# Optimization experiments

Measured on AMD Instinct MI355X. Metric: run time of the kernel, lower is better.

## Reference

```python
import jax, jax.numpy as jnp
import numpy as np

D_MODEL = 1024
N_HEAD = 16
N_KV_HEAD = 4
D_K = D_MODEL // N_HEAD          # 64
N_REP = N_HEAD // N_KV_HEAD      # 4
B, S = 2, 2048


def setup_inputs() -> dict:
    key = jax.random.key(0)
    ks = jax.random.split(key, 7)
    scale = 1.0 / np.sqrt(D_MODEL)
    return {
        "q": jax.random.normal(ks[0], (B, S, D_MODEL), jnp.float32),
        "k": jax.random.normal(ks[1], (B, S, D_MODEL), jnp.float32),
        "v": jax.random.normal(ks[2], (B, S, D_MODEL), jnp.float32),
        # weights stored [in, out] (nn.Linear applies x @ W.T; we fold the transpose)
        "W_q": jax.random.normal(ks[3], (D_MODEL, N_HEAD * D_K), jnp.float32) * scale,
        "W_k": jax.random.normal(ks[4], (D_MODEL, N_KV_HEAD * D_K), jnp.float32) * scale,
        "W_v": jax.random.normal(ks[5], (D_MODEL, N_KV_HEAD * D_K), jnp.float32) * scale,
        "W_o": jax.random.normal(ks[6], (D_MODEL, D_MODEL), jnp.float32) * scale,
    }


def reference(q, k, v, W_q, W_k, W_v, W_o):
    batch, seq_q, _ = q.shape
    seq_k = k.shape[1]
    # projections -> [b, h, s, d]
    Q = (q @ W_q).reshape(batch, seq_q, N_HEAD, D_K).transpose(0, 2, 1, 3)
    K = (k @ W_k).reshape(batch, seq_k, N_KV_HEAD, D_K).transpose(0, 2, 1, 3)
    V = (v @ W_v).reshape(batch, seq_k, N_KV_HEAD, D_K).transpose(0, 2, 1, 3)
    # repeat each KV head n_rep times consecutively (matches expand+reshape)
    K = jnp.repeat(K, N_REP, axis=1)  # [b, n_head, seq_k, d_k]
    V = jnp.repeat(V, N_REP, axis=1)
    scores = jnp.einsum('bhqd,bhkd->bhqk', Q, K) / np.sqrt(D_K).astype(jnp.float32)
    attn = jax.nn.softmax(scores, axis=-1)
    out = jnp.einsum('bhqk,bhkd->bhqd', attn, V)  # [b, h, seq_q, d_k]
    out = out.transpose(0, 2, 1, 3).reshape(batch, seq_q, D_MODEL)
    return out @ W_o
```

## Files before the change

### kernel.cpp

```cpp
#include <hip/hip_runtime.h>
#include <hip/hip_bf16.h>
#include <stdint.h>

#define DEVINL __device__ __forceinline__

typedef unsigned short u16;
typedef __bf16 bf16x8 __attribute__((ext_vector_type(8)));
typedef float f32x4 __attribute__((ext_vector_type(4)));
typedef float f32x16 __attribute__((ext_vector_type(16)));
typedef unsigned short u16x8 __attribute__((ext_vector_type(8)));
typedef unsigned int u32x4 __attribute__((ext_vector_type(4)));

constexpr int BATCH = 2, SEQ = 2048, DM = 1024, NH = 16, NKVH = 4, DK = 64;
#define QSCALE 0.18033688f

DEVINL u16 f2bf(float f) {
    unsigned u = __builtin_bit_cast(unsigned, f);
    u += 0x7fffu + ((u >> 16) & 1u);
    return (u16)(u >> 16);
}

DEVINL unsigned pkbf(float a, float b) {
    unsigned r;
    asm("v_cvt_pk_bf16_f32 %0, %1, %2" : "=v"(r) : "v"(a), "v"(b));
    return r;
}
DEVINL void swap32(unsigned& a, unsigned& b) {
    asm("v_permlane32_swap_b32 %0, %1" : "+v"(a), "+v"(b));
}
DEVINL float fexp2(float x) {
    float r;
    asm("v_exp_f32 %0, %1" : "=v"(r) : "v"(x));
    return r;
}

DEVINL void gload16(const void* g, void* l) {
    __builtin_amdgcn_global_load_lds(
        (const __attribute__((address_space(1))) unsigned int*)g,
        (__attribute__((address_space(3))) unsigned int*)l, 16, 0, 0);
}

DEVINL bf16x8 ldfrag(const u16* p) { return *reinterpret_cast<const bf16x8*>(p); }

__global__ __launch_bounds__(256) void prep_kernel(
    const float* __restrict__ Wq, const float* __restrict__ Wk,
    const float* __restrict__ Wv, const float* __restrict__ Wo,
    u16* __restrict__ Wqt, u16* __restrict__ Wkt,
    u16* __restrict__ Wvt, u16* __restrict__ Wot) {
    __shared__ float tile[32][33];
    int bid = blockIdx.x;
    int z = bid >> 10, rem = bid & 1023;
    const float* W;
    u16* Wt;
    int N;
    switch (z) {
        case 0: W = Wq; Wt = Wqt; N = 1024; break;
        case 1: W = Wk; Wt = Wkt; N = 256; break;
        case 2: W = Wv; Wt = Wvt; N = 256; break;
        default: W = Wo; Wt = Wot; N = 1024; break;
    }
    int n0 = (rem & 31) * 32;
    if (n0 >= N) return;
    int k0 = (rem >> 5) * 32;
    int tx = threadIdx.x & 31, ty = threadIdx.x >> 5;
#pragma unroll
    for (int r = 0; r < 4; ++r)
        tile[ty + 8 * r][tx] = W[(size_t)(k0 + ty + 8 * r) * N + n0 + tx];
    __syncthreads();
#pragma unroll
    for (int r = 0; r < 4; ++r)
        Wt[(size_t)(n0 + ty + 8 * r) * 1024 + k0 + tx] = f2bf(tile[tx][ty + 8 * r]);
}

#define GEMM_CORE64(Apt, Bpt)                                                 \
    __shared__ __align__(16) u16 Al[2][128 * 64];                             \
    __shared__ __align__(16) u16 Bl[2][64 * 64];                              \
    const int tid = threadIdx.x;                                              \
    const int lane = tid & 63;                                                \
    const int w = tid >> 6;                                                   \
    const u16* Ab = (Apt) + (size_t)m0 * 1024;                                \
    const u16* Bb = (Bpt) + (size_t)n0 * 1024;                                \
    f32x4 acc[2][4] = {};                                                     \
    auto stage = [&](int buf, int kt) {                                       \
        _Pragma("unroll") for (int rnd = 0; rnd < 4; ++rnd) {                 \
            int L = tid * 16 + rnd * 4096;                                    \
            int row = L >> 7;                                                 \
            int cb = (L & 127) ^ ((row & 7) << 4);                            \
            gload16(Ab + (size_t)row * 1024 + kt * 64 + (cb >> 1),            \
                    &Al[buf][L >> 1]);                                        \
        }                                                                     \
        _Pragma("unroll") for (int rnd = 0; rnd < 2; ++rnd) {                 \
            int L = tid * 16 + rnd * 4096;                                    \
            int row = L >> 7;                                                 \
            int cb = (L & 127) ^ ((row & 7) << 4);                            \
            gload16(Bb + (size_t)row * 1024 + kt * 64 + (cb >> 1),            \
                    &Bl[buf][L >> 1]);                                        \
        }                                                                     \
    };                                                                        \
    stage(0, 0);                                                              \
    __syncthreads();                                                          \
    int buf = 0;                                                              \
    for (int kt = 0; kt < 16; ++kt) {                                         \
        if (kt + 1 < 16) stage(buf ^ 1, kt + 1);                              \
        bf16x8 af[2][2], bfr[2][4];                                           \
        _Pragma("unroll") for (int kk = 0; kk < 2; ++kk)                      \
            _Pragma("unroll") for (int mi = 0; mi < 2; ++mi) {                \
                int row = w * 32 + mi * 16 + (lane & 15);                     \
                int cb = (kk * 64 + (lane >> 4) * 16) ^ ((row & 7) << 4);     \
                af[kk][mi] = ldfrag(&Al[buf][row * 64 + (cb >> 1)]);          \
            }                                                                 \
        _Pragma("unroll") for (int kk = 0; kk < 2; ++kk)                      \
            _Pragma("unroll") for (int ni = 0; ni < 4; ++ni) {                \
                int row = ni * 16 + (lane & 15);                              \
                int cb = (kk * 64 + (lane >> 4) * 16) ^ ((row & 7) << 4);     \
                bfr[kk][ni] = ldfrag(&Bl[buf][row * 64 + (cb >> 1)]);         \
            }                                                                 \
        _Pragma("unroll") for (int kk = 0; kk < 2; ++kk)                      \
            _Pragma("unroll") for (int mi = 0; mi < 2; ++mi)                  \
                _Pragma("unroll") for (int ni = 0; ni < 4; ++ni)              \
                    acc[mi][ni] = __builtin_amdgcn_mfma_f32_16x16x32_bf16(    \
                        af[kk][mi], bfr[kk][ni], acc[mi][ni], 0, 0, 0);       \
        __syncthreads();                                                      \
        buf ^= 1;                                                             \
    }

__global__ __launch_bounds__(256) void proj_kernel(
    const float* __restrict__ q32, const float* __restrict__ k32, const float* __restrict__ v32,
    const u16* __restrict__ Wqt, const u16* __restrict__ Wkt, const u16* __restrict__ Wvt,
    u16* __restrict__ Qp, u16* __restrict__ Kf, u16* __restrict__ Vf) {
    int bid = blockIdx.x;
    int tile = (bid & 7) * 96 + (bid >> 3);
    const float* A32;
    const u16* Bt;
    int m0, n0, z;
    if (tile < 512) {
        z = 0; A32 = q32; Bt = Wqt; m0 = (tile >> 4) * 128; n0 = (tile & 15) * 64;
    } else if (tile < 640) {
        int t = tile - 512;
        z = 1; A32 = k32; Bt = Wkt; m0 = (t >> 2) * 128; n0 = (t & 3) * 64;
    } else {
        int t = tile - 640;
        z = 2; A32 = v32; Bt = Wvt; m0 = (t >> 2) * 128; n0 = (t & 3) * 64;
    }

    __shared__ __align__(16) u16 Al[2][128 * 64];
    __shared__ __align__(16) u16 Bl[2][64 * 64];
    const int tid = threadIdx.x;
    const int lane = tid & 63;
    const int w = tid >> 6;
    const float* Ab32 = A32 + (size_t)m0 * 1024;
    const u16* Bb = Bt + (size_t)n0 * 1024;
    f32x4 acc[2][4] = {};

    int arow[4], adst[4];
    const float* asrc[4];
#pragma unroll
    for (int rnd = 0; rnd < 4; ++rnd) {
        int L = tid * 16 + rnd * 4096;
        int row = L >> 7, colb = L & 127;
        arow[rnd] = row;
        adst[rnd] = (row * 128 + (colb ^ ((row & 7) << 4)));
        asrc[rnd] = Ab32 + (size_t)row * 1024 + (colb >> 1);
    }
    const int LB = tid * 16;
    const int brow0 = LB >> 7;
    const int bcb0 = (LB & 127) ^ ((brow0 & 7) << 4);
    const int LB1 = LB + 4096;
    const int brow1 = LB1 >> 7;
    const int bcb1 = (LB1 & 127) ^ ((brow1 & 7) << 4);

    auto stageB = [&](int buf, int kt) {
        gload16(Bb + (size_t)brow0 * 1024 + kt * 64 + (bcb0 >> 1), &Bl[buf][LB >> 1]);
        gload16(Bb + (size_t)brow1 * 1024 + kt * 64 + (bcb1 >> 1), &Bl[buf][LB1 >> 1]);
    };
    auto packwr = [&](int buf, const float4& a, const float4& b, int dst) {
        u32x4 pk;
        pk[0] = pkbf(a.x, a.y); pk[1] = pkbf(a.z, a.w);
        pk[2] = pkbf(b.x, b.y); pk[3] = pkbf(b.z, b.w);
        *(u32x4*)((char*)&Al[buf][0] + dst) = pk;
    };

    {
        stageB(0, 0);
#pragma unroll
        for (int rnd = 0; rnd < 4; ++rnd) {
            float4 a = *(const float4*)asrc[rnd];
            float4 b = *(const float4*)(asrc[rnd] + 4);
            packwr(0, a, b, adst[rnd]);
        }
    }
    __syncthreads();

    int buf = 0;
    for (int kt = 0; kt < 16; ++kt) {
        float4 a4[4], b4[4];
        if (kt + 1 < 16) {
            stageB(buf ^ 1, kt + 1);
#pragma unroll
            for (int rnd = 0; rnd < 4; ++rnd) {
                const float* s = asrc[rnd] + (kt + 1) * 64;
                a4[rnd] = *(const float4*)s;
                b4[rnd] = *(const float4*)(s + 4);
            }
        }
        bf16x8 af[2][2], bfr[2][4];
#pragma unroll
        for (int kk = 0; kk < 2; ++kk)
#pragma unroll
            for (int mi = 0; mi < 2; ++mi) {
                int row = w * 32 + mi * 16 + (lane & 15);
                int cb = (kk * 64 + (lane >> 4) * 16) ^ ((row & 7) << 4);
                af[kk][mi] = ldfrag(&Al[buf][row * 64 + (cb >> 1)]);
            }
#pragma unroll
        for (int kk = 0; kk < 2; ++kk)
#pragma unroll
            for (int ni = 0; ni < 4; ++ni) {
                int row = ni * 16 + (lane & 15);
                int cb = (kk * 64 + (lane >> 4) * 16) ^ ((row & 7) << 4);
                bfr[kk][ni] = ldfrag(&Bl[buf][row * 64 + (cb >> 1)]);
            }
#pragma unroll
        for (int kk = 0; kk < 2; ++kk)
#pragma unroll
            for (int mi = 0; mi < 2; ++mi)
#pragma unroll
                for (int ni = 0; ni < 4; ++ni)
                    acc[mi][ni] = __builtin_amdgcn_mfma_f32_16x16x32_bf16(
                        af[kk][mi], bfr[kk][ni], acc[mi][ni], 0, 0, 0);
        if (kt + 1 < 16) {
#pragma unroll
            for (int rnd = 0; rnd < 4; ++rnd)
                packwr(buf ^ 1, a4[rnd], b4[rnd], adst[rnd]);
        }
        __syncthreads();
        buf ^= 1;
    }

#pragma unroll
    for (int mi = 0; mi < 2; ++mi)
#pragma unroll
        for (int ni = 0; ni < 4; ++ni)
#pragma unroll
            for (int r = 0; r < 4; ++r) {
                int row = m0 + w * 32 + mi * 16 + (lane >> 4) * 4 + r;
                int col = n0 + ni * 16 + (lane & 15);
                float v = acc[mi][ni][r];
                int bb = row >> 11, s = row & 2047;
                int hh = col >> 6, dd = col & 63;
                if (z == 0) {
                    Qp[((((size_t)bb * NH + hh) * 2048 + s) << 6) + dd] = f2bf(v * QSCALE);
                } else if (z == 1) {
                    size_t base = (size_t)(bb * NKVH + hh) * 131072;
                    int s32 = s >> 5, q31s = s & 31;
                    int c = dd >> 4, hib = (dd >> 3) & 1, j = dd & 7;
                    Kf[base + (size_t)((s32 * 4 + c) * 64 + hib * 32 + q31s) * 8 + j] = f2bf(v);
                } else {
                    size_t base = (size_t)(bb * NKVH + hh) * 131072;
                    int kt = s >> 6, i = (s >> 4) & 3, hib = (s >> 3) & 1, j = s & 7;
                    int dt = dd >> 5, q31v = dd & 31;
                    Vf[base + (size_t)((((kt * 2 + dt) * 4 + i) * 64) + hib * 32 + q31v) * 8 + j] = f2bf(v);
                }
            }
}

__global__ __launch_bounds__(256) void oproj_kernel(const u16* __restrict__ Oa,
                                                    const u16* __restrict__ Wot,
                                                    float* __restrict__ out) {
    int bid = blockIdx.x;
    int tile = (bid & 7) * 64 + (bid >> 3);
    const int m0 = (tile >> 4) * 128, n0 = (tile & 15) * 64;

    GEMM_CORE64(Oa, Wot)

#pragma unroll
    for (int mi = 0; mi < 2; ++mi)
#pragma unroll
        for (int ni = 0; ni < 4; ++ni)
#pragma unroll
            for (int r = 0; r < 4; ++r) {
                int row = m0 + w * 32 + mi * 16 + (lane >> 4) * 4 + r;
                int col = n0 + ni * 16 + (lane & 15);
                out[(size_t)row * 1024 + col] = acc[mi][ni][r];
            }
}

__global__ __launch_bounds__(256) void attn_kernel(const u16* __restrict__ Qp,
                                                   const u16* __restrict__ Kf,
                                                   const u16* __restrict__ Vf,
                                                   u16* __restrict__ Oa) {
    __shared__ __align__(16) u16 Kl[4][4096];
    __shared__ __align__(16) u16 Vl[4][4096];

    const int tid = threadIdx.x;
    const int lane = tid & 63, w = tid >> 6;
    const int hi = lane >> 5, q31 = lane & 31;
    const int qt = blockIdx.x, h = blockIdx.y, b = blockIdx.z;
    const int kvh = h >> 2;
    const int qrow = qt * 128 + w * 32 + q31;

    const u16* Qb = Qp + ((size_t)((b * NH + h) * SEQ) + qrow) * 64 + hi * 8;
    bf16x8 qf0 = ldfrag(Qb), qf1 = ldfrag(Qb + 16);
    bf16x8 qf2 = ldfrag(Qb + 32), qf3 = ldfrag(Qb + 48);

    const u16* KbG = Kf + (size_t)(b * NKVH + kvh) * 131072;
    const u16* VbG = Vf + (size_t)(b * NKVH + kvh) * 131072;

    auto stageT = [&](int slot, int tile) {
        const u16* Kg = KbG + (size_t)tile * 4096 + lane * 8;
        const u16* Vg = VbG + (size_t)tile * 4096 + lane * 8;
        gload16(Kg + w * 512, &Kl[slot][w * 512]);
        gload16(Kg + (w + 4) * 512, &Kl[slot][(w + 4) * 512]);
        gload16(Vg + w * 512, &Vl[slot][w * 512]);
        gload16(Vg + (w + 4) * 512, &Vl[slot][(w + 4) * 512]);
    };

    f32x16 od0 = {}, od1 = {};
    float lsum = 0.f;
    f32x16 sA0 = {}, sA1 = {}, sB0 = {}, sB1 = {};
    bf16x8 kA[8], kB[8], vf[8];

    stageT(0, 0);
    stageT(1, 1);
    stageT(2, 2);
    asm volatile("s_waitcnt vmcnt(0)" ::: "memory");
    __builtin_amdgcn_s_barrier();

#pragma unroll
    for (int r = 0; r < 8; ++r) kA[r] = ldfrag(&Kl[0][r * 512 + lane * 8]);
    sA0 = __builtin_amdgcn_mfma_f32_32x32x16_bf16(kA[0], qf0, sA0, 0, 0, 0);
    sA0 = __builtin_amdgcn_mfma_f32_32x32x16_bf16(kA[1], qf1, sA0, 0, 0, 0);
    sA0 = __builtin_amdgcn_mfma_f32_32x32x16_bf16(kA[2], qf2, sA0, 0, 0, 0);
    sA0 = __builtin_amdgcn_mfma_f32_32x32x16_bf16(kA[3], qf3, sA0, 0, 0, 0);
    sA1 = __builtin_amdgcn_mfma_f32_32x32x16_bf16(kA[4], qf0, sA1, 0, 0, 0);
    sA1 = __builtin_amdgcn_mfma_f32_32x32x16_bf16(kA[5], qf1, sA1, 0, 0, 0);
    sA1 = __builtin_amdgcn_mfma_f32_32x32x16_bf16(kA[6], qf2, sA1, 0, 0, 0);
    sA1 = __builtin_amdgcn_mfma_f32_32x32x16_bf16(kA[7], qf3, sA1, 0, 0, 0);
#pragma unroll
    for (int r = 0; r < 8; ++r) kB[r] = ldfrag(&Kl[1][r * 512 + lane * 8]);
#pragma unroll
    for (int r = 0; r < 8; ++r) vf[r] = ldfrag(&Vl[0][r * 512 + lane * 8]);

#define PACKP(sv, s, outf)                                    \
        {                                                     \
            unsigned x0 = pkbf(sv[8 * s + 0], sv[8 * s + 1]); \
            unsigned x1 = pkbf(sv[8 * s + 2], sv[8 * s + 3]); \
            unsigned y0 = pkbf(sv[8 * s + 4], sv[8 * s + 5]); \
            unsigned y1 = pkbf(sv[8 * s + 6], sv[8 * s + 7]); \
            swap32(x0, y0);                                   \
            swap32(x1, y1);                                   \
            u32x4 tt2 = {x0, x1, y0, y1};                     \
            outf = __builtin_bit_cast(bf16x8, tt2);           \
        }

#define BODY(SC0, SC1, SN0, SN1, KQK, KLD, T)                                 \
    {                                                                         \
        stageT(((T) + 3) & 3, ((T) + 3) & 31);                                \
        __builtin_amdgcn_s_setprio(1);                                        \
        SN0 = {};                                                             \
        SN1 = {};                                                             \
        SN0 = __builtin_amdgcn_mfma_f32_32x32x16_bf16(KQK[0], qf0, SN0, 0, 0, 0); \
        SN0 = __builtin_amdgcn_mfma_f32_32x32x16_bf16(KQK[1], qf1, SN0, 0, 0, 0); \
        SN0 = __builtin_amdgcn_mfma_f32_32x32x16_bf16(KQK[2], qf2, SN0, 0, 0, 0); \
        SN0 = __builtin_amdgcn_mfma_f32_32x32x16_bf16(KQK[3], qf3, SN0, 0, 0, 0); \
        SN1 = __builtin_amdgcn_mfma_f32_32x32x16_bf16(KQK[4], qf0, SN1, 0, 0, 0); \
        SN1 = __builtin_amdgcn_mfma_f32_32x32x16_bf16(KQK[5], qf1, SN1, 0, 0, 0); \
        SN1 = __builtin_amdgcn_mfma_f32_32x32x16_bf16(KQK[6], qf2, SN1, 0, 0, 0); \
        SN1 = __builtin_amdgcn_mfma_f32_32x32x16_bf16(KQK[7], qf3, SN1, 0, 0, 0); \
        __builtin_amdgcn_s_setprio(0);                                        \
        {                                                                     \
            const u16* Ksl = &Kl[((T) + 2) & 3][lane * 8];                    \
            _Pragma("unroll") for (int r = 0; r < 8; ++r)                     \
                KLD[r] = ldfrag(Ksl + r * 512);                               \
        }                                                                     \
        _Pragma("unroll") for (int r = 0; r < 16; ++r) {                      \
            SC0[r] = fexp2(SC0[r]);                                           \
            SC1[r] = fexp2(SC1[r]);                                           \
        }                                                                     \
        {                                                                     \
            f32x16 ts = SC0 + SC1;                                            \
            float u0 = (ts[0] + ts[1]) + (ts[2] + ts[3]);                     \
            float u1 = (ts[4] + ts[5]) + (ts[6] + ts[7]);                     \
            float u2 = (ts[8] + ts[9]) + (ts[10] + ts[11]);                   \
            float u3 = (ts[12] + ts[13]) + (ts[14] + ts[15]);                 \
            lsum += (u0 + u1) + (u2 + u3);                                    \
        }                                                                     \
        bf16x8 pa0, pa1, pa2, pa3;                                            \
        PACKP(SC0, 0, pa0)                                                    \
        PACKP(SC0, 1, pa1)                                                    \
        PACKP(SC1, 0, pa2)                                                    \
        PACKP(SC1, 1, pa3)                                                    \
        __builtin_amdgcn_s_setprio(1);                                        \
        od0 = __builtin_amdgcn_mfma_f32_32x32x16_bf16(vf[0], pa0, od0, 0, 0, 0); \
        od0 = __builtin_amdgcn_mfma_f32_32x32x16_bf16(vf[1], pa1, od0, 0, 0, 0); \
        od0 = __builtin_amdgcn_mfma_f32_32x32x16_bf16(vf[2], pa2, od0, 0, 0, 0); \
        od0 = __builtin_amdgcn_mfma_f32_32x32x16_bf16(vf[3], pa3, od0, 0, 0, 0); \
        od1 = __builtin_amdgcn_mfma_f32_32x32x16_bf16(vf[4], pa0, od1, 0, 0, 0); \
        od1 = __builtin_amdgcn_mfma_f32_32x32x16_bf16(vf[5], pa1, od1, 0, 0, 0); \
        od1 = __builtin_amdgcn_mfma_f32_32x32x16_bf16(vf[6], pa2, od1, 0, 0, 0); \
        od1 = __builtin_amdgcn_mfma_f32_32x32x16_bf16(vf[7], pa3, od1, 0, 0, 0); \
        __builtin_amdgcn_s_setprio(0);                                        \
        {                                                                     \
            const u16* Vsl = &Vl[((T) + 1) & 3][lane * 8];                    \
            _Pragma("unroll") for (int r = 0; r < 8; ++r)                     \
                vf[r] = ldfrag(Vsl + r * 512);                                \
        }                                                                     \
        asm volatile("s_waitcnt vmcnt(0)" ::: "memory");                      \
        __builtin_amdgcn_s_barrier();                                         \
    }

    for (int tt = 0; tt < 16; ++tt) {
        int t = tt * 2;
        BODY(sA0, sA1, sB0, sB1, kB, kA, t)
        BODY(sB0, sB1, sA0, sA1, kA, kB, t + 1)
    }
#undef BODY
#undef PACKP

    lsum += __shfl_xor(lsum, 32);

    float inv = 1.0f / lsum;
    u16* Ob = Oa + ((size_t)(b * SEQ) + qrow) * DM + h * 64;
#pragma unroll
    for (int i = 0; i < 8; ++i) {
        int r = 2 * i;
        int d = (r & 3) + 8 * (r >> 2) + 4 * hi;
        *(unsigned*)(Ob + d) = pkbf(od0[r] * inv, od0[r + 1] * inv);
        *(unsigned*)(Ob + 32 + d) = pkbf(od1[r] * inv, od1[r + 1] * inv);
    }
}

extern "C" void kernel_launch(void* const* d_in, const int* in_sizes, int n_in,
                              void* d_out, int out_size, void* d_ws, size_t ws_size,
                              hipStream_t stream) {
    const float* q  = (const float*)d_in[0];
    const float* k  = (const float*)d_in[1];
    const float* v  = (const float*)d_in[2];
    const float* Wq = (const float*)d_in[3];
    const float* Wk = (const float*)d_in[4];
    const float* Wv = (const float*)d_in[5];
    const float* Wo = (const float*)d_in[6];
    float* out = (float*)d_out;

    char* ws = (char*)d_ws;
    u16* Wqt = (u16*)(ws + (size_t)0);
    u16* Wkt = (u16*)(ws + ((size_t)2 << 20));
    u16* Wvt = (u16*)(ws + ((size_t)3 << 20));
    u16* Wot = (u16*)(ws + ((size_t)4 << 20));
    u16* Qp  = (u16*)(ws + ((size_t)6 << 20));
    u16* Kf  = (u16*)(ws + ((size_t)14 << 20));
    u16* Vf  = (u16*)(ws + ((size_t)16 << 20));
    u16* Oa  = (u16*)(ws + ((size_t)18 << 20));

    prep_kernel<<<4096, 256, 0, stream>>>(Wq, Wk, Wv, Wo, Wqt, Wkt, Wvt, Wot);

    proj_kernel<<<768, 256, 0, stream>>>(q, k, v, Wqt, Wkt, Wvt, Qp, Kf, Vf);

    attn_kernel<<<dim3(16, 16, 2), 256, 0, stream>>>(Qp, Kf, Vf, Oa);

    oproj_kernel<<<512, 256, 0, stream>>>(Oa, Wot, out);
}
```

Measured before the change: 119.1 us.

## Load K/V fragments directly from global and compute row sums via MFMA

The attention kernel drops the LDS staging ring with its per-tile barriers and loads K and V fragments straight from global memory into registers, one tile ahead. The softmax denominator is now taken from an MFMA against a ones vector on the bf16 probabilities, replacing the scalar add reduction and the cross-lane shuffle. This removes LDS traffic and block-wide synchronisation. In exchange, the four waves now fetch identical K/V data separately (relying on cache), global latency is exposed with only one tile of prefetch, and the row sum uses the rounded bf16 probabilities.

```diff
diff --git a/kernel.cpp b/kernel.cpp
--- a/kernel.cpp
+++ b/kernel.cpp
@@ -152,13 +152,12 @@
     const u16* Bb = Bt + (size_t)n0 * 1024;
     f32x4 acc[2][4] = {};
 
-    int arow[4], adst[4];
+    int adst[4];
     const float* asrc[4];
 #pragma unroll
     for (int rnd = 0; rnd < 4; ++rnd) {
         int L = tid * 16 + rnd * 4096;
         int row = L >> 7, colb = L & 127;
-        arow[rnd] = row;
         adst[rnd] = (row * 128 + (colb ^ ((row & 7) << 4)));
         asrc[rnd] = Ab32 + (size_t)row * 1024 + (colb >> 1);
     }
@@ -289,9 +288,6 @@
                                                    const u16* __restrict__ Kf,
                                                    const u16* __restrict__ Vf,
                                                    u16* __restrict__ Oa) {
-    __shared__ __align__(16) u16 Kl[4][4096];
-    __shared__ __align__(16) u16 Vl[4][4096];
-
     const int tid = threadIdx.x;
     const int lane = tid & 63, w = tid >> 6;
     const int hi = lane >> 5, q31 = lane & 31;
@@ -303,43 +299,33 @@
     bf16x8 qf0 = ldfrag(Qb), qf1 = ldfrag(Qb + 16);
     bf16x8 qf2 = ldfrag(Qb + 32), qf3 = ldfrag(Qb + 48);
 
-    const u16* KbG = Kf + (size_t)(b * NKVH + kvh) * 131072;
-    const u16* VbG = Vf + (size_t)(b * NKVH + kvh) * 131072;
-
-    auto stageT = [&](int slot, int tile) {
-        const u16* Kg = KbG + (size_t)tile * 4096 + lane * 8;
-        const u16* Vg = VbG + (size_t)tile * 4096 + lane * 8;
-        gload16(Kg + w * 512, &Kl[slot][w * 512]);
-        gload16(Kg + (w + 4) * 512, &Kl[slot][(w + 4) * 512]);
-        gload16(Vg + w * 512, &Vl[slot][w * 512]);
-        gload16(Vg + (w + 4) * 512, &Vl[slot][(w + 4) * 512]);
-    };
-
-    f32x16 od0 = {}, od1 = {};
-    float lsum = 0.f;
+    const u16* Kb = Kf + (size_t)(b * NKVH + kvh) * 131072 + lane * 8;
+    const u16* Vb = Vf + (size_t)(b * NKVH + kvh) * 131072 + lane * 8;
+
+    bf16x8 k0[8], k1[8], vf[8];
+#pragma unroll
+    for (int r = 0; r < 8; ++r) k0[r] = ldfrag(Kb + (size_t)r * 512);
+#pragma unroll
+    for (int r = 0; r < 8; ++r) k1[r] = ldfrag(Kb + (size_t)(8 + r) * 512);
+#pragma unroll
+    for (int r = 0; r < 8; ++r) vf[r] = ldfrag(Vb + (size_t)r * 512);
+
+    u16x8 ov;
+#pragma unroll
+    for (int j = 0; j < 8; ++j) ov[j] = 0x3F80;
+    const bf16x8 ones = __builtin_bit_cast(bf16x8, ov);
+
+    f32x16 od0 = {}, od1 = {}, lacc = {};
     f32x16 sA0 = {}, sA1 = {}, sB0 = {}, sB1 = {};
-    bf16x8 kA[8], kB[8], vf[8];
-
-    stageT(0, 0);
-    stageT(1, 1);
-    stageT(2, 2);
-    asm volatile("s_waitcnt vmcnt(0)" ::: "memory");
-    __builtin_amdgcn_s_barrier();
-
-#pragma unroll
-    for (int r = 0; r < 8; ++r) kA[r] = ldfrag(&Kl[0][r * 512 + lane * 8]);
-    sA0 = __builtin_amdgcn_mfma_f32_32x32x16_bf16(kA[0], qf0, sA0, 0, 0, 0);
-    sA0 = __builtin_amdgcn_mfma_f32_32x32x16_bf16(kA[1], qf1, sA0, 0, 0, 0);
-    sA0 = __builtin_amdgcn_mfma_f32_32x32x16_bf16(kA[2], qf2, sA0, 0, 0, 0);
-    sA0 = __builtin_amdgcn_mfma_f32_32x32x16_bf16(kA[3], qf3, sA0, 0, 0, 0);
-    sA1 = __builtin_amdgcn_mfma_f32_32x32x16_bf16(kA[4], qf0, sA1, 0, 0, 0);
-    sA1 = __builtin_amdgcn_mfma_f32_32x32x16_bf16(kA[5], qf1, sA1, 0, 0, 0);
-    sA1 = __builtin_amdgcn_mfma_f32_32x32x16_bf16(kA[6], qf2, sA1, 0, 0, 0);
-    sA1 = __builtin_amdgcn_mfma_f32_32x32x16_bf16(kA[7], qf3, sA1, 0, 0, 0);
-#pragma unroll
-    for (int r = 0; r < 8; ++r) kB[r] = ldfrag(&Kl[1][r * 512 + lane * 8]);
-#pragma unroll
-    for (int r = 0; r < 8; ++r) vf[r] = ldfrag(&Vl[0][r * 512 + lane * 8]);
+
+    sA0 = __builtin_amdgcn_mfma_f32_32x32x16_bf16(k0[0], qf0, sA0, 0, 0, 0);
+    sA0 = __builtin_amdgcn_mfma_f32_32x32x16_bf16(k0[1], qf1, sA0, 0, 0, 0);
+    sA0 = __builtin_amdgcn_mfma_f32_32x32x16_bf16(k0[2], qf2, sA0, 0, 0, 0);
+    sA0 = __builtin_amdgcn_mfma_f32_32x32x16_bf16(k0[3], qf3, sA0, 0, 0, 0);
+    sA1 = __builtin_amdgcn_mfma_f32_32x32x16_bf16(k0[4], qf0, sA1, 0, 0, 0);
+    sA1 = __builtin_amdgcn_mfma_f32_32x32x16_bf16(k0[5], qf1, sA1, 0, 0, 0);
+    sA1 = __builtin_amdgcn_mfma_f32_32x32x16_bf16(k0[6], qf2, sA1, 0, 0, 0);
+    sA1 = __builtin_amdgcn_mfma_f32_32x32x16_bf16(k0[7], qf3, sA1, 0, 0, 0);
 
 #define PACKP(sv, s, outf)                                    \
         {                                                     \
@@ -353,9 +339,8 @@
             outf = __builtin_bit_cast(bf16x8, tt2);           \
         }
 
-#define BODY(SC0, SC1, SN0, SN1, KQK, KLD, T)                                 \
+#define BODY(SC0, SC1, SN0, SN1, KQK, KLD, KIDX, VIDX)                        \
     {                                                                         \
-        stageT(((T) + 3) & 3, ((T) + 3) & 31);                                \
         __builtin_amdgcn_s_setprio(1);                                        \
         SN0 = {};                                                             \
         SN1 = {};                                                             \
@@ -368,22 +353,11 @@
         SN1 = __builtin_amdgcn_mfma_f32_32x32x16_bf16(KQK[6], qf2, SN1, 0, 0, 0); \
         SN1 = __builtin_amdgcn_mfma_f32_32x32x16_bf16(KQK[7], qf3, SN1, 0, 0, 0); \
         __builtin_amdgcn_s_setprio(0);                                        \
-        {                                                                     \
-            const u16* Ksl = &Kl[((T) + 2) & 3][lane * 8];                    \
-            _Pragma("unroll") for (int r = 0; r < 8; ++r)                     \
-                KLD[r] = ldfrag(Ksl + r * 512);                               \
-        }                                                                     \
+        _Pragma("unroll") for (int r = 0; r < 8; ++r)                         \
+            KLD[r] = ldfrag(Kb + (size_t)((KIDX) * 8 + r) * 512);             \
         _Pragma("unroll") for (int r = 0; r < 16; ++r) {                      \
             SC0[r] = fexp2(SC0[r]);                                           \
             SC1[r] = fexp2(SC1[r]);                                           \
-        }                                                                     \
-        {                                                                     \
-            f32x16 ts = SC0 + SC1;                                            \
-            float u0 = (ts[0] + ts[1]) + (ts[2] + ts[3]);                     \
-            float u1 = (ts[4] + ts[5]) + (ts[6] + ts[7]);                     \
-            float u2 = (ts[8] + ts[9]) + (ts[10] + ts[11]);                   \
-            float u3 = (ts[12] + ts[13]) + (ts[14] + ts[15]);                 \
-            lsum += (u0 + u1) + (u2 + u3);                                    \
         }                                                                     \
         bf16x8 pa0, pa1, pa2, pa3;                                            \
         PACKP(SC0, 0, pa0)                                                    \
@@ -391,6 +365,10 @@
         PACKP(SC1, 0, pa2)                                                    \
         PACKP(SC1, 1, pa3)                                                    \
         __builtin_amdgcn_s_setprio(1);                                        \
+        lacc = __builtin_amdgcn_mfma_f32_32x32x16_bf16(ones, pa0, lacc, 0, 0, 0); \
+        lacc = __builtin_amdgcn_mfma_f32_32x32x16_bf16(ones, pa1, lacc, 0, 0, 0); \
+        lacc = __builtin_amdgcn_mfma_f32_32x32x16_bf16(ones, pa2, lacc, 0, 0, 0); \
+        lacc = __builtin_amdgcn_mfma_f32_32x32x16_bf16(ones, pa3, lacc, 0, 0, 0); \
         od0 = __builtin_amdgcn_mfma_f32_32x32x16_bf16(vf[0], pa0, od0, 0, 0, 0); \
         od0 = __builtin_amdgcn_mfma_f32_32x32x16_bf16(vf[1], pa1, od0, 0, 0, 0); \
         od0 = __builtin_amdgcn_mfma_f32_32x32x16_bf16(vf[2], pa2, od0, 0, 0, 0); \
@@ -400,26 +378,19 @@
         od1 = __builtin_amdgcn_mfma_f32_32x32x16_bf16(vf[6], pa2, od1, 0, 0, 0); \
         od1 = __builtin_amdgcn_mfma_f32_32x32x16_bf16(vf[7], pa3, od1, 0, 0, 0); \
         __builtin_amdgcn_s_setprio(0);                                        \
-        {                                                                     \
-            const u16* Vsl = &Vl[((T) + 1) & 3][lane * 8];                    \
-            _Pragma("unroll") for (int r = 0; r < 8; ++r)                     \
-                vf[r] = ldfrag(Vsl + r * 512);                                \
-        }                                                                     \
-        asm volatile("s_waitcnt vmcnt(0)" ::: "memory");                      \
-        __builtin_amdgcn_s_barrier();                                         \
+        _Pragma("unroll") for (int r = 0; r < 8; ++r)                         \
+            vf[r] = ldfrag(Vb + (size_t)((VIDX) * 8 + r) * 512);              \
     }
 
     for (int tt = 0; tt < 16; ++tt) {
         int t = tt * 2;
-        BODY(sA0, sA1, sB0, sB1, kB, kA, t)
-        BODY(sB0, sB1, sA0, sA1, kA, kB, t + 1)
+        BODY(sA0, sA1, sB0, sB1, k1, k0, (t + 2) & 31, (t + 1) & 31)
+        BODY(sB0, sB1, sA0, sA1, k0, k1, (t + 3) & 31, (t + 2) & 31)
     }
 #undef BODY
 #undef PACKP
 
-    lsum += __shfl_xor(lsum, 32);
-
-    float inv = 1.0f / lsum;
+    float inv = 1.0f / lacc[0];
     u16* Ob = Oa + ((size_t)(b * SEQ) + qrow) * DM + h * 64;
 #pragma unroll
     for (int i = 0; i < 8; ++i) {
```

After: 103.4 us. 13.2% less time.
